# Kernel optimization log

Hardware: AMD Instinct MI355X
Metric: run time of the kernel (lower is better)

Reference implementation:

```python
import jax, jax.numpy as jnp
import numpy as np

D_MODEL = 1024
N_HEADS = 16
D_K = D_MODEL // N_HEADS
D_FF = 4096
EPS = 1e-5


def layer_norm(x, gamma, beta):
    mu = jnp.mean(x, axis=-1, keepdims=True)
    var = jnp.var(x, axis=-1, keepdims=True)
    return (x - mu) * jax.lax.rsqrt(var + EPS) * gamma + beta


def setup_inputs() -> dict:
    key = jax.random.key(0)
    ks = jax.random.split(key, 16)
    B, S = 4, 1024
    s = 0.02
    inp = {
        "x": jax.random.normal(ks[0], (B, S, D_MODEL), dtype=jnp.float32),
        "mask": jnp.ones((B, 1, 1, S), dtype=jnp.int32),
        "Wq": jax.random.normal(ks[1], (D_MODEL, D_MODEL), jnp.float32) * s,
        "bq": jnp.zeros((D_MODEL,), jnp.float32),
        "Wk": jax.random.normal(ks[2], (D_MODEL, D_MODEL), jnp.float32) * s,
        "bk": jnp.zeros((D_MODEL,), jnp.float32),
        "Wv": jax.random.normal(ks[3], (D_MODEL, D_MODEL), jnp.float32) * s,
        "bv": jnp.zeros((D_MODEL,), jnp.float32),
        "Wo": jax.random.normal(ks[4], (D_MODEL, D_MODEL), jnp.float32) * s,
        "bo": jnp.zeros((D_MODEL,), jnp.float32),
        "W1": jax.random.normal(ks[5], (D_MODEL, D_FF), jnp.float32) * s,
        "b1": jnp.zeros((D_FF,), jnp.float32),
        "W2": jax.random.normal(ks[6], (D_FF, D_MODEL), jnp.float32) * s,
        "b2": jnp.zeros((D_MODEL,), jnp.float32),
        "ln1_g": jnp.ones((D_MODEL,), jnp.float32),
        "ln1_b": jnp.zeros((D_MODEL,), jnp.float32),
        "ln2_g": jnp.ones((D_MODEL,), jnp.float32),
        "ln2_b": jnp.zeros((D_MODEL,), jnp.float32),
    }
    return inp


def reference(x, mask, Wq, bq, Wk, bk, Wv, bv, Wo, bo, W1, b1, W2, b2,
              ln1_g, ln1_b, ln2_g, ln2_b):
    B, S, _ = x.shape
    # QKV projections -> [B, H, S, d_k]
    def split_heads(t):
        return t.reshape(B, S, N_HEADS, D_K).transpose(0, 2, 1, 3)
    Q = split_heads(x @ Wq + bq)
    K = split_heads(x @ Wk + bk)
    V = split_heads(x @ Wv + bv)
    # scores [B, H, S, S]
    scores = jnp.einsum('bhqd,bhkd->bhqk', Q, K) / jnp.sqrt(jnp.float32(D_K))
    scores = jnp.where(mask == 0, jnp.float32(-1e9), scores)
    attn = jax.nn.softmax(scores, axis=-1)
    ctx = jnp.einsum('bhqk,bhkd->bhqd', attn, V)
    ctx = ctx.transpose(0, 2, 1, 3).reshape(B, S, D_MODEL)
    attn_out = ctx @ Wo + bo
    # residual + LN (dropout is identity in eval)
    h = layer_norm(x + attn_out, ln1_g, ln1_b)
    ff = jax.nn.relu(h @ W1 + b1) @ W2 + b2
    return layer_norm(h + ff, ln2_g, ln2_b)
```

## Files before the change

### kernel.cpp

```cpp
#include <hip/hip_runtime.h>
#include <hip/hip_bf16.h>

typedef __attribute__((ext_vector_type(8))) short bf16x8;
typedef __attribute__((ext_vector_type(4))) short bf16x4;
typedef __attribute__((ext_vector_type(4))) float f32x4;
typedef unsigned int u32;
typedef unsigned short ush;

#define SEQ 1024
#define NH 16
#define MTOT 4096

__device__ __forceinline__ ush f2bf(float f){
  u32 u = __float_as_uint(f);
  u32 r = (u + 0x7fffu + ((u >> 16) & 1u)) >> 16;
  return (ush)r;
}

__device__ __forceinline__ f32x4 mfma16(bf16x8 a, bf16x8 b, f32x4 c){
  return __builtin_amdgcn_mfma_f32_16x16x32_bf16(a, b, c, 0, 0, 0);
}

__device__ __forceinline__ void gload_lds16(const ush* g, ush* l){
  __builtin_amdgcn_global_load_lds(
      (const __attribute__((address_space(1))) u32*)g,
      (__attribute__((address_space(3))) u32*)l, 16, 0, 0);
}

__global__ __launch_bounds__(256) void cvt_kernel(const float* __restrict__ src,
                                                  ush* __restrict__ dst, int n){
  int i = (blockIdx.x * 256 + threadIdx.x) * 4;
  if (i < n){
    float4 v = *(const float4*)&src[i];
    ushort4 o = { f2bf(v.x), f2bf(v.y), f2bf(v.z), f2bf(v.w) };
    *(ushort4*)&dst[i] = o;
  }
}

__global__ __launch_bounds__(256) void tconv_kernel(const float* __restrict__ src,
                                                    ush* __restrict__ dst, int R, int C){
  __shared__ float t[32][33];
  int tx = threadIdx.x & 31, ty = threadIdx.x >> 5;
  int r0 = blockIdx.y * 32, c0 = blockIdx.x * 32;
  #pragma unroll
  for (int i = 0; i < 32; i += 8)
    t[ty + i][tx] = src[(size_t)(r0 + ty + i) * C + (c0 + tx)];
  __syncthreads();
  #pragma unroll
  for (int i = 0; i < 32; i += 8)
    dst[(size_t)(c0 + ty + i) * R + (r0 + tx)] = f2bf(t[tx][ty + i]);
}

__global__ __launch_bounds__(256) void biaspack_kernel(const float* __restrict__ bq,
    const float* __restrict__ bk, const float* __restrict__ bv, float* __restrict__ dst){
  int i = blockIdx.x * 256 + threadIdx.x;
  if (i < 3072){
    float v = (i < 1024) ? bq[i] : (i < 2048) ? bk[i - 1024] : bv[i - 2048];
    dst[i] = v;
  }
}

template<bool RELU, bool OUTF32>
__global__ __launch_bounds__(256) void gemm_kernel(
    const ush* __restrict__ A, const ush* __restrict__ Bt,
    const float* __restrict__ bias,
    float* __restrict__ Cf, ush* __restrict__ Cb,
    int M, int N, int K, int ldc)
{
  __shared__ ush As[128 * 32];
  __shared__ ush Bs[128 * 32];
  const int tid = threadIdx.x;
  const int lane = tid & 63, wid = tid >> 6;
  const int g = lane >> 4, qr = lane & 15;
  const int bm = blockIdx.y * 128, bn = blockIdx.x * 128;
  const int srow = lane >> 2, scol = (lane & 3) * 8;
  const ush* aA0 = A  + (size_t)(bm + wid * 16 + srow) * K + scol;
  const ush* aB0 = Bt + (size_t)(bn + wid * 16 + srow) * K + scol;
  const ush* aA1 = aA0 + (size_t)64 * K;
  const ush* aB1 = aB0 + (size_t)64 * K;
  ush* lA0 = As + wid * 512;
  ush* lA1 = As + (4 + wid) * 512;
  ush* lB0 = Bs + wid * 512;
  ush* lB1 = Bs + (4 + wid) * 512;
  const int wm = (wid >> 1) * 64, wn = (wid & 1) * 64;
  f32x4 acc[4][4] = {};
  for (int kt = 0; kt < K; kt += 32){
    __syncthreads();
    gload_lds16(aA0 + kt, lA0);
    gload_lds16(aA1 + kt, lA1);
    gload_lds16(aB0 + kt, lB0);
    gload_lds16(aB1 + kt, lB1);
    __syncthreads();
    bf16x8 af[4], bfr[4];
    #pragma unroll
    for (int i = 0; i < 4; i++){
      af[i]  = *(const bf16x8*)(As + (wm + i * 16 + qr) * 32 + g * 8);
      bfr[i] = *(const bf16x8*)(Bs + (wn + i * 16 + qr) * 32 + g * 8);
    }
    #pragma unroll
    for (int i = 0; i < 4; i++)
      #pragma unroll
      for (int j = 0; j < 4; j++)
        acc[i][j] = mfma16(af[i], bfr[j], acc[i][j]);
  }
  const int row0 = bm + wm + g * 4;
  const int col0 = bn + wn + qr;
  #pragma unroll
  for (int j = 0; j < 4; j++){
    const int col = col0 + j * 16;
    const float bv = bias[col];
    #pragma unroll
    for (int i = 0; i < 4; i++){
      #pragma unroll
      for (int r = 0; r < 4; r++){
        float v = acc[i][j][r] + bv;
        if (RELU) v = fmaxf(v, 0.f);
        const size_t idx = (size_t)(row0 + i * 16 + r) * ldc + col;
        if (OUTF32) Cf[idx] = v; else Cb[idx] = f2bf(v);
      }
    }
  }
}

__global__ __launch_bounds__(256) void attn_kernel(
    const ush* __restrict__ qkv, const int* __restrict__ mask,
    ush* __restrict__ ctx)
{
  __shared__ ush Vt[64 * 40];
  __shared__ ush Pl[4][16 * 40];
  __shared__ int mk[1024];
  const int tid = threadIdx.x;
  const int lane = tid & 63, w = tid >> 6;
  const int g = lane >> 4, qr = lane & 15;
  const int hb = blockIdx.y;
  const int b = hb >> 4, hh = hb & 15;
  const int qt = blockIdx.x;

  { int4 mv = *(const int4*)&mask[b * SEQ + tid * 4]; *(int4*)&mk[tid * 4] = mv; }
  __syncthreads();

  const size_t rowQ = (size_t)(b * SEQ + qt * 64 + w * 16 + qr);
  const ush* Qp = qkv + rowQ * 3072 + hh * 64;
  bf16x8 qf0 = *(const bf16x8*)(Qp + g * 8);
  bf16x8 qf1 = *(const bf16x8*)(Qp + 32 + g * 8);

  const ush* Kb = qkv + (size_t)b * SEQ * 3072 + 1024 + hh * 64;
  const ush* Vb = qkv + (size_t)b * SEQ * 3072 + 2048 + hh * 64;

  f32x4 oa[4] = {};
  float m_run = -1e30f, l_run = 0.f;
  const int vkey = tid >> 3, vd0 = (tid & 7) * 8;

  for (int kt = 0; kt < SEQ / 32; ++kt){
    const int k0 = kt * 32;
    bf16x8 vv = *(const bf16x8*)(Vb + (size_t)(k0 + vkey) * 3072 + vd0);
    const ush* Kr0 = Kb + (size_t)(k0 + qr) * 3072;
    const ush* Kr1 = Kr0 + (size_t)16 * 3072;
    bf16x8 ka0 = *(const bf16x8*)(Kr0 + g * 8);
    bf16x8 ka1 = *(const bf16x8*)(Kr0 + 32 + g * 8);
    bf16x8 kb0 = *(const bf16x8*)(Kr1 + g * 8);
    bf16x8 kb1 = *(const bf16x8*)(Kr1 + 32 + g * 8);
    f32x4 z = {0.f, 0.f, 0.f, 0.f};
    f32x4 st0 = mfma16(ka0, qf0, z); st0 = mfma16(ka1, qf1, st0);
    f32x4 st1 = mfma16(kb0, qf0, z); st1 = mfma16(kb1, qf1, st1);
    float sc[8];
    #pragma unroll
    for (int r = 0; r < 4; r++){
      int key = k0 + g * 4 + r;
      sc[r]     = (mk[key] == 0)      ? -1e9f : st0[r] * 0.125f;
      sc[4 + r] = (mk[key + 16] == 0) ? -1e9f : st1[r] * 0.125f;
    }
    float pm = sc[0];
    #pragma unroll
    for (int r = 1; r < 8; r++) pm = fmaxf(pm, sc[r]);
    pm = fmaxf(pm, __shfl_xor(pm, 16));
    pm = fmaxf(pm, __shfl_xor(pm, 32));
    float m_new = fmaxf(m_run, pm);
    float corr = __expf(m_run - m_new);
    float ls = 0.f;
    #pragma unroll
    for (int r = 0; r < 8; r++){ sc[r] = __expf(sc[r] - m_new); ls += sc[r]; }
    ls += __shfl_xor(ls, 16); ls += __shfl_xor(ls, 32);
    l_run = l_run * corr + ls; m_run = m_new;
    #pragma unroll
    for (int r = 0; r < 4; r++){
      float cr = __shfl(corr, g * 4 + r);
      oa[0][r] *= cr; oa[1][r] *= cr; oa[2][r] *= cr; oa[3][r] *= cr;
    }
    bf16x4 p0, p1;
    #pragma unroll
    for (int r = 0; r < 4; r++){ p0[r] = (short)f2bf(sc[r]); p1[r] = (short)f2bf(sc[4 + r]); }
    *(bf16x4*)&Pl[w][qr * 40 + g * 4]      = p0;
    *(bf16x4*)&Pl[w][qr * 40 + 16 + g * 4] = p1;
    __syncthreads();
    #pragma unroll
    for (int j = 0; j < 8; j++) Vt[(vd0 + j) * 40 + vkey] = (ush)vv[j];
    __syncthreads();
    bf16x8 pf = *(const bf16x8*)&Pl[w][qr * 40 + g * 8];
    #pragma unroll
    for (int d = 0; d < 4; d++){
      bf16x8 vf = *(const bf16x8*)&Vt[(d * 16 + qr) * 40 + g * 8];
      oa[d] = mfma16(pf, vf, oa[d]);
    }
  }
  float linv = 1.f / l_run;
  #pragma unroll
  for (int r = 0; r < 4; r++){
    float lr = __shfl(linv, g * 4 + r);
    size_t rowO = (size_t)(b * SEQ + qt * 64 + w * 16 + g * 4 + r);
    #pragma unroll
    for (int d = 0; d < 4; d++)
      ctx[rowO * 1024 + hh * 64 + d * 16 + qr] = f2bf(oa[d][r] * lr);
  }
}

template<bool WB>
__global__ __launch_bounds__(256) void ln_kernel(
    const float* __restrict__ X, const float* __restrict__ Y,
    const float* __restrict__ gam, const float* __restrict__ bet,
    float* __restrict__ Of, ush* __restrict__ Ob)
{
  const int row = blockIdx.x, tid = threadIdx.x;
  const size_t base = (size_t)row * 1024 + tid * 4;
  float4 xv = *(const float4*)&X[base];
  float4 yv = *(const float4*)&Y[base];
  float s0 = xv.x + yv.x, s1 = xv.y + yv.y, s2 = xv.z + yv.z, s3 = xv.w + yv.w;
  float sum = s0 + s1 + s2 + s3;
  float sq  = s0 * s0 + s1 * s1 + s2 * s2 + s3 * s3;
  #pragma unroll
  for (int o = 1; o < 64; o <<= 1){ sum += __shfl_xor(sum, o); sq += __shfl_xor(sq, o); }
  __shared__ float red[8];
  int lane = tid & 63, w = tid >> 6;
  if (lane == 0){ red[w] = sum; red[4 + w] = sq; }
  __syncthreads();
  sum = red[0] + red[1] + red[2] + red[3];
  sq  = red[4] + red[5] + red[6] + red[7];
  float mean = sum * (1.f / 1024.f);
  float var  = sq * (1.f / 1024.f) - mean * mean;
  float rs = rsqrtf(var + 1e-5f);
  float4 gv = *(const float4*)&gam[tid * 4];
  float4 bv = *(const float4*)&bet[tid * 4];
  float o0 = (s0 - mean) * rs * gv.x + bv.x;
  float o1 = (s1 - mean) * rs * gv.y + bv.y;
  float o2 = (s2 - mean) * rs * gv.z + bv.z;
  float o3 = (s3 - mean) * rs * gv.w + bv.w;
  float4 ov = { o0, o1, o2, o3 };
  *(float4*)&Of[base] = ov;
  if (WB){
    ushort4 ob = { f2bf(o0), f2bf(o1), f2bf(o2), f2bf(o3) };
    *(ushort4*)&Ob[base] = ob;
  }
}

extern "C" void kernel_launch(void* const* d_in, const int* in_sizes, int n_in,
                              void* d_out, int out_size, void* d_ws, size_t ws_size,
                              hipStream_t stream)
{
  const float* x    = (const float*)d_in[0];
  const int*   mask = (const int*)  d_in[1];
  const float* Wq = (const float*)d_in[2];
  const float* bq = (const float*)d_in[3];
  const float* Wk = (const float*)d_in[4];
  const float* bk = (const float*)d_in[5];
  const float* Wv = (const float*)d_in[6];
  const float* bv = (const float*)d_in[7];
  const float* Wo = (const float*)d_in[8];
  const float* bo = (const float*)d_in[9];
  const float* W1 = (const float*)d_in[10];
  const float* b1 = (const float*)d_in[11];
  const float* W2 = (const float*)d_in[12];
  const float* b2 = (const float*)d_in[13];
  const float* g1 = (const float*)d_in[14];
  const float* be1= (const float*)d_in[15];
  const float* g2 = (const float*)d_in[16];
  const float* be2= (const float*)d_in[17];
  float* out = (float*)d_out;

  char* ws = (char*)d_ws;
  size_t off = 0;
  auto alloc = [&](size_t bytes)->void*{ void* p = ws + off; off += (bytes + 255) & ~(size_t)255; return p; };
  ush* xb     = (ush*)alloc((size_t)MTOT * 1024 * 2);
  ush* wqkvT  = (ush*)alloc((size_t)3072 * 1024 * 2);
  ush* woT    = (ush*)alloc((size_t)1024 * 1024 * 2);
  ush* w1T    = (ush*)alloc((size_t)4096 * 1024 * 2);
  ush* w2T    = (ush*)alloc((size_t)1024 * 4096 * 2);
  float* bqkv = (float*)alloc(3072 * 4);
  ush* qkv    = (ush*)alloc((size_t)MTOT * 3072 * 2);
  ush* ctx    = (ush*)alloc((size_t)MTOT * 1024 * 2);
  float* attn_out = (float*)alloc((size_t)MTOT * 1024 * 4);
  float* h    = (float*)alloc((size_t)MTOT * 1024 * 4);
  ush* hb     = (ush*)alloc((size_t)MTOT * 1024 * 2);
  ush* ff1    = qkv;
  float* ff2  = attn_out;

  cvt_kernel<<<dim3(4096), dim3(256), 0, stream>>>(x, xb, MTOT * 1024);
  tconv_kernel<<<dim3(32, 32), dim3(256), 0, stream>>>(Wq, wqkvT,                 1024, 1024);
  tconv_kernel<<<dim3(32, 32), dim3(256), 0, stream>>>(Wk, wqkvT + 1024 * 1024,   1024, 1024);
  tconv_kernel<<<dim3(32, 32), dim3(256), 0, stream>>>(Wv, wqkvT + 2048 * 1024,   1024, 1024);
  tconv_kernel<<<dim3(32, 32), dim3(256), 0, stream>>>(Wo, woT,                   1024, 1024);
  tconv_kernel<<<dim3(128, 32), dim3(256), 0, stream>>>(W1, w1T, 1024, 4096);
  tconv_kernel<<<dim3(32, 128), dim3(256), 0, stream>>>(W2, w2T, 4096, 1024);
  biaspack_kernel<<<dim3(12), dim3(256), 0, stream>>>(bq, bk, bv, bqkv);

  gemm_kernel<false, false><<<dim3(24, 32), dim3(256), 0, stream>>>(
      xb, wqkvT, bqkv, nullptr, qkv, MTOT, 3072, 1024, 3072);

  attn_kernel<<<dim3(16, 64), dim3(256), 0, stream>>>(qkv, mask, ctx);

  gemm_kernel<false, true><<<dim3(8, 32), dim3(256), 0, stream>>>(
      ctx, woT, bo, attn_out, nullptr, MTOT, 1024, 1024, 1024);

  ln_kernel<true><<<dim3(4096), dim3(256), 0, stream>>>(x, attn_out, g1, be1, h, hb);

  gemm_kernel<true, false><<<dim3(32, 32), dim3(256), 0, stream>>>(
      hb, w1T, b1, nullptr, ff1, MTOT, 4096, 1024, 4096);

  gemm_kernel<false, true><<<dim3(8, 32), dim3(256), 0, stream>>>(
      ff1, w2T, b2, ff2, nullptr, MTOT, 1024, 4096, 1024);

  ln_kernel<false><<<dim3(4096), dim3(256), 0, stream>>>(h, ff2, g2, be2, out, nullptr);
}
```

Before: 463.4 us.

## Replace GEMMs with 256x256 pipelined swizzled kernel plus split-K reduced in layernorm

Swaps the 128x128 single-buffered GEMM for a 512-thread 256x256 tile kernel. It uses double-buffered LDS with XOR-swizzled layout, phase barriers with setprio, and a grid swizzle for L2 locality. The two N=1024 GEMMs are split along K into 4 partial fp32 buffers. The layernorm kernel sums those partials and adds the bias, so the reduction is fused there. This targets low MFMA utilization and LDS/global-load latency, and it adds wave count to the small GEMMs. The cost is extra partial-sum traffic and higher register and LDS pressure.

Result: faster. 416.6 us (-10.1%).

```diff
diff --git a/kernel.cpp b/kernel.cpp
--- a/kernel.cpp
+++ b/kernel.cpp
@@ -8,7 +8,6 @@
 typedef unsigned short ush;
 
 #define SEQ 1024
-#define NH 16
 #define MTOT 4096
 
 __device__ __forceinline__ ush f2bf(float f){
@@ -60,63 +59,146 @@
   }
 }
 
-template<bool RELU, bool OUTF32>
-__global__ __launch_bounds__(256) void gemm_kernel(
+__device__ __forceinline__ void stage_piece(ush* piece, const ush* g0, int K,
+                                            int tid, int w){
+  #pragma unroll
+  for (int I = 0; I < 2; I++){
+    int c = I * 512 + tid;
+    int r = c >> 2;
+    int gl = (c & 3) ^ ((r >> 1) & 3);
+    gload_lds16(g0 + (size_t)r * K + gl * 8, piece + I * 4096 + w * 512);
+  }
+}
+
+__device__ __forceinline__ bf16x8 frag(const ush* piece, int row, int g){
+  int phys = g ^ ((row >> 1) & 3);
+  return *(const bf16x8*)(piece + row * 32 + phys * 8);
+}
+
+#define PH_BAR_TOP() do{ __builtin_amdgcn_sched_barrier(0); \
+  __builtin_amdgcn_s_barrier(); \
+  asm volatile("s_waitcnt lgkmcnt(0)" ::: "memory"); \
+  __builtin_amdgcn_sched_barrier(0); \
+  __builtin_amdgcn_s_setprio(1); }while(0)
+#define PH_BAR_BOT() do{ __builtin_amdgcn_s_setprio(0); \
+  __builtin_amdgcn_sched_barrier(0); \
+  __builtin_amdgcn_s_barrier(); }while(0)
+
+template<int RELU, int OUTF32>
+__global__ __launch_bounds__(512, 2) void gemm8_kernel(
     const ush* __restrict__ A, const ush* __restrict__ Bt,
     const float* __restrict__ bias,
-    float* __restrict__ Cf, ush* __restrict__ Cb,
-    int M, int N, int K, int ldc)
+    ush* __restrict__ Cb, float* __restrict__ Cf,
+    int M, int N, int K, int ldc, int ksl)
 {
-  __shared__ ush As[128 * 32];
-  __shared__ ush Bs[128 * 32];
+  __shared__ ush lds[2][2][2][8192];
   const int tid = threadIdx.x;
-  const int lane = tid & 63, wid = tid >> 6;
+  const int lane = tid & 63, w = tid >> 6;
   const int g = lane >> 4, qr = lane & 15;
-  const int bm = blockIdx.y * 128, bn = blockIdx.x * 128;
-  const int srow = lane >> 2, scol = (lane & 3) * 8;
-  const ush* aA0 = A  + (size_t)(bm + wid * 16 + srow) * K + scol;
-  const ush* aB0 = Bt + (size_t)(bn + wid * 16 + srow) * K + scol;
-  const ush* aA1 = aA0 + (size_t)64 * K;
-  const ush* aB1 = aB0 + (size_t)64 * K;
-  ush* lA0 = As + wid * 512;
-  ush* lA1 = As + (4 + wid) * 512;
-  ush* lB0 = Bs + wid * 512;
-  ush* lB1 = Bs + (4 + wid) * 512;
-  const int wm = (wid >> 1) * 64, wn = (wid & 1) * 64;
-  f32x4 acc[4][4] = {};
-  for (int kt = 0; kt < K; kt += 32){
-    __syncthreads();
-    gload_lds16(aA0 + kt, lA0);
-    gload_lds16(aA1 + kt, lA1);
-    gload_lds16(aB0 + kt, lB0);
-    gload_lds16(aB1 + kt, lB1);
-    __syncthreads();
+  const int wr = w >> 2, wc = w & 3;
+  const int gx = gridDim.x;
+  const int nwg = gx * gridDim.y;
+  const int id = blockIdx.y * gx + blockIdx.x;
+  const int swz = (id & 7) * (nwg >> 3) + (id >> 3);
+  const int bn = (swz % gx) * 256;
+  const int bm = (swz / gx) * 256;
+  const int kbase = blockIdx.z * ksl;
+  const int NT = ksl >> 6;
+  const ush* Ab = A  + (size_t)bm * K + kbase;
+  const ush* Bb = Bt + (size_t)bn * K + kbase;
+
+  stage_piece(lds[0][0][0], Ab,      K, tid, w);
+  stage_piece(lds[0][1][0], Bb,      K, tid, w);
+  stage_piece(lds[0][0][1], Ab + 32, K, tid, w);
+  stage_piece(lds[0][1][1], Bb + 32, K, tid, w);
+  if (NT > 1){
+    stage_piece(lds[1][0][0], Ab + 64, K, tid, w);
+    stage_piece(lds[1][1][0], Bb + 64, K, tid, w);
+  }
+  asm volatile("s_waitcnt vmcnt(4)" ::: "memory");
+  __builtin_amdgcn_sched_barrier(0);
+  __builtin_amdgcn_s_barrier();
+
+  f32x4 acc[8][4] = {};
+  const int ar = wr * 128 + qr;
+  const int br = wc * 64 + qr;
+
+  for (int T = 0; T < NT; ++T){
+    const int cb = T & 1, nb = cb ^ 1;
+    const ush* An = Ab + (size_t)(T + 1) * 64;
+    const ush* Bn = Bb + (size_t)(T + 1) * 64;
+    const ush* Af = Ab + (size_t)(T + 2) * 64;
+    const ush* Bf = Bb + (size_t)(T + 2) * 64;
     bf16x8 af[4], bfr[4];
-    #pragma unroll
-    for (int i = 0; i < 4; i++){
-      af[i]  = *(const bf16x8*)(As + (wm + i * 16 + qr) * 32 + g * 8);
-      bfr[i] = *(const bf16x8*)(Bs + (wn + i * 16 + qr) * 32 + g * 8);
-    }
+
+    #pragma unroll
+    for (int j = 0; j < 4; j++) bfr[j] = frag(lds[cb][1][0], br + j * 16, g);
+    #pragma unroll
+    for (int i = 0; i < 4; i++) af[i] = frag(lds[cb][0][0], ar + i * 16, g);
+    if (T + 1 < NT) stage_piece(lds[nb][0][1], An + 32, K, tid, w);
+    PH_BAR_TOP();
     #pragma unroll
     for (int i = 0; i < 4; i++)
       #pragma unroll
       for (int j = 0; j < 4; j++)
         acc[i][j] = mfma16(af[i], bfr[j], acc[i][j]);
-  }
-  const int row0 = bm + wm + g * 4;
-  const int col0 = bn + wn + qr;
+    PH_BAR_BOT();
+
+    #pragma unroll
+    for (int i = 0; i < 4; i++) af[i] = frag(lds[cb][0][0], ar + 64 + i * 16, g);
+    if (T + 1 < NT) stage_piece(lds[nb][1][1], Bn + 32, K, tid, w);
+    PH_BAR_TOP();
+    #pragma unroll
+    for (int i = 0; i < 4; i++)
+      #pragma unroll
+      for (int j = 0; j < 4; j++)
+        acc[4 + i][j] = mfma16(af[i], bfr[j], acc[4 + i][j]);
+    PH_BAR_BOT();
+
+    #pragma unroll
+    for (int j = 0; j < 4; j++) bfr[j] = frag(lds[cb][1][1], br + j * 16, g);
+    #pragma unroll
+    for (int i = 0; i < 4; i++) af[i] = frag(lds[cb][0][1], ar + i * 16, g);
+    if (T + 2 < NT) stage_piece(lds[cb][0][0], Af, K, tid, w);
+    PH_BAR_TOP();
+    #pragma unroll
+    for (int i = 0; i < 4; i++)
+      #pragma unroll
+      for (int j = 0; j < 4; j++)
+        acc[i][j] = mfma16(af[i], bfr[j], acc[i][j]);
+    PH_BAR_BOT();
+
+    #pragma unroll
+    for (int i = 0; i < 4; i++) af[i] = frag(lds[cb][0][1], ar + 64 + i * 16, g);
+    if (T + 2 < NT) stage_piece(lds[cb][1][0], Bf, K, tid, w);
+    PH_BAR_TOP();
+    #pragma unroll
+    for (int i = 0; i < 4; i++)
+      #pragma unroll
+      for (int j = 0; j < 4; j++)
+        acc[4 + i][j] = mfma16(af[i], bfr[j], acc[4 + i][j]);
+    __builtin_amdgcn_s_setprio(0);
+    __builtin_amdgcn_sched_barrier(0);
+    asm volatile("s_waitcnt vmcnt(4)" ::: "memory");
+    __builtin_amdgcn_sched_barrier(0);
+    __builtin_amdgcn_s_barrier();
+  }
+
+  float* Cfz = Cf;
+  if (OUTF32) Cfz = Cf + (size_t)blockIdx.z * M * ldc;
   #pragma unroll
   for (int j = 0; j < 4; j++){
-    const int col = col0 + j * 16;
-    const float bv = bias[col];
-    #pragma unroll
-    for (int i = 0; i < 4; i++){
+    const int col = bn + wc * 64 + j * 16 + qr;
+    const float bv = OUTF32 ? 0.f : bias[col];
+    #pragma unroll
+    for (int i = 0; i < 8; i++){
+      const int row0 = bm + wr * 128 + i * 16 + g * 4;
       #pragma unroll
-      for (int r = 0; r < 4; r++){
-        float v = acc[i][j][r] + bv;
+      for (int rr = 0; rr < 4; rr++){
+        float v = acc[i][j][rr] + bv;
         if (RELU) v = fmaxf(v, 0.f);
-        const size_t idx = (size_t)(row0 + i * 16 + r) * ldc + col;
-        if (OUTF32) Cf[idx] = v; else Cb[idx] = f2bf(v);
+        const size_t idx = (size_t)(row0 + rr) * ldc + col;
+        if (OUTF32) Cfz[idx] = v; else Cb[idx] = f2bf(v);
       }
     }
   }
@@ -215,16 +297,22 @@
 }
 
 template<bool WB>
-__global__ __launch_bounds__(256) void ln_kernel(
-    const float* __restrict__ X, const float* __restrict__ Y,
+__global__ __launch_bounds__(256) void ln4_kernel(
+    const float* __restrict__ X, const float* __restrict__ P,
+    const float* __restrict__ bias,
     const float* __restrict__ gam, const float* __restrict__ bet,
     float* __restrict__ Of, ush* __restrict__ Ob)
 {
   const int row = blockIdx.x, tid = threadIdx.x;
   const size_t base = (size_t)row * 1024 + tid * 4;
   float4 xv = *(const float4*)&X[base];
-  float4 yv = *(const float4*)&Y[base];
-  float s0 = xv.x + yv.x, s1 = xv.y + yv.y, s2 = xv.z + yv.z, s3 = xv.w + yv.w;
+  float4 bv4 = *(const float4*)&bias[tid * 4];
+  float s0 = xv.x + bv4.x, s1 = xv.y + bv4.y, s2 = xv.z + bv4.z, s3 = xv.w + bv4.w;
+  #pragma unroll
+  for (int z = 0; z < 4; z++){
+    float4 p = *(const float4*)&P[(size_t)z * 4194304 + base];
+    s0 += p.x; s1 += p.y; s2 += p.z; s3 += p.w;
+  }
   float sum = s0 + s1 + s2 + s3;
   float sq  = s0 * s0 + s1 * s1 + s2 * s2 + s3 * s3;
   #pragma unroll
@@ -239,11 +327,11 @@
   float var  = sq * (1.f / 1024.f) - mean * mean;
   float rs = rsqrtf(var + 1e-5f);
   float4 gv = *(const float4*)&gam[tid * 4];
-  float4 bv = *(const float4*)&bet[tid * 4];
-  float o0 = (s0 - mean) * rs * gv.x + bv.x;
-  float o1 = (s1 - mean) * rs * gv.y + bv.y;
-  float o2 = (s2 - mean) * rs * gv.z + bv.z;
-  float o3 = (s3 - mean) * rs * gv.w + bv.w;
+  float4 bt = *(const float4*)&bet[tid * 4];
+  float o0 = (s0 - mean) * rs * gv.x + bt.x;
+  float o1 = (s1 - mean) * rs * gv.y + bt.y;
+  float o2 = (s2 - mean) * rs * gv.z + bt.z;
+  float o3 = (s3 - mean) * rs * gv.w + bt.w;
   float4 ov = { o0, o1, o2, o3 };
   *(float4*)&Of[base] = ov;
   if (WB){
@@ -287,36 +375,35 @@
   float* bqkv = (float*)alloc(3072 * 4);
   ush* qkv    = (ush*)alloc((size_t)MTOT * 3072 * 2);
   ush* ctx    = (ush*)alloc((size_t)MTOT * 1024 * 2);
-  float* attn_out = (float*)alloc((size_t)MTOT * 1024 * 4);
+  float* part = (float*)alloc((size_t)4 * MTOT * 1024 * 4);
   float* h    = (float*)alloc((size_t)MTOT * 1024 * 4);
   ush* hb     = (ush*)alloc((size_t)MTOT * 1024 * 2);
   ush* ff1    = qkv;
-  float* ff2  = attn_out;
 
   cvt_kernel<<<dim3(4096), dim3(256), 0, stream>>>(x, xb, MTOT * 1024);
-  tconv_kernel<<<dim3(32, 32), dim3(256), 0, stream>>>(Wq, wqkvT,                 1024, 1024);
-  tconv_kernel<<<dim3(32, 32), dim3(256), 0, stream>>>(Wk, wqkvT + 1024 * 1024,   1024, 1024);
-  tconv_kernel<<<dim3(32, 32), dim3(256), 0, stream>>>(Wv, wqkvT + 2048 * 1024,   1024, 1024);
-  tconv_kernel<<<dim3(32, 32), dim3(256), 0, stream>>>(Wo, woT,                   1024, 1024);
+  tconv_kernel<<<dim3(32, 32), dim3(256), 0, stream>>>(Wq, wqkvT,               1024, 1024);
+  tconv_kernel<<<dim3(32, 32), dim3(256), 0, stream>>>(Wk, wqkvT + 1024 * 1024, 1024, 1024);
+  tconv_kernel<<<dim3(32, 32), dim3(256), 0, stream>>>(Wv, wqkvT + 2048 * 1024, 1024, 1024);
+  tconv_kernel<<<dim3(32, 32), dim3(256), 0, stream>>>(Wo, woT,                 1024, 1024);
   tconv_kernel<<<dim3(128, 32), dim3(256), 0, stream>>>(W1, w1T, 1024, 4096);
   tconv_kernel<<<dim3(32, 128), dim3(256), 0, stream>>>(W2, w2T, 4096, 1024);
   biaspack_kernel<<<dim3(12), dim3(256), 0, stream>>>(bq, bk, bv, bqkv);
 
-  gemm_kernel<false, false><<<dim3(24, 32), dim3(256), 0, stream>>>(
-      xb, wqkvT, bqkv, nullptr, qkv, MTOT, 3072, 1024, 3072);
+  gemm8_kernel<0, 0><<<dim3(12, 16, 1), dim3(512), 0, stream>>>(
+      xb, wqkvT, bqkv, qkv, nullptr, MTOT, 3072, 1024, 3072, 1024);
 
   attn_kernel<<<dim3(16, 64), dim3(256), 0, stream>>>(qkv, mask, ctx);
 
-  gemm_kernel<false, true><<<dim3(8, 32), dim3(256), 0, stream>>>(
-      ctx, woT, bo, attn_out, nullptr, MTOT, 1024, 1024, 1024);
-
-  ln_kernel<true><<<dim3(4096), dim3(256), 0, stream>>>(x, attn_out, g1, be1, h, hb);
-
-  gemm_kernel<true, false><<<dim3(32, 32), dim3(256), 0, stream>>>(
-      hb, w1T, b1, nullptr, ff1, MTOT, 4096, 1024, 4096);
-
-  gemm_kernel<false, true><<<dim3(8, 32), dim3(256), 0, stream>>>(
-      ff1, w2T, b2, ff2, nullptr, MTOT, 1024, 4096, 1024);
-
-  ln_kernel<false><<<dim3(4096), dim3(256), 0, stream>>>(h, ff2, g2, be2, out, nullptr);
-}
+  gemm8_kernel<0, 1><<<dim3(4, 16, 4), dim3(512), 0, stream>>>(
+      ctx, woT, nullptr, nullptr, part, MTOT, 1024, 1024, 1024, 256);
+
+  ln4_kernel<true><<<dim3(4096), dim3(256), 0, stream>>>(x, part, bo, g1, be1, h, hb);
+
+  gemm8_kernel<1, 0><<<dim3(16, 16, 1), dim3(512), 0, stream>>>(
+      hb, w1T, b1, ff1, nullptr, MTOT, 4096, 1024, 4096, 1024);
+
+  gemm8_kernel<0, 1><<<dim3(4, 16, 4), dim3(512), 0, stream>>>(
+      ff1, w2T, nullptr, nullptr, part, MTOT, 1024, 4096, 1024, 1024);
+
+  ln4_kernel<false><<<dim3(4096), dim3(256), 0, stream>>>(h, part, b2, g2, be2, out, nullptr);
+}
```
